# Kernel tuning notes

Hardware: AMD Instinct MI355X
Metric: run time of the kernel (lower is better)

The kernel has to match this reference:

```python
import jax, jax.numpy as jnp
import numpy as np
from jax import lax

K = 3            # kernel_size
PAD = (K - 1) // 2


def zero_insert_stride2(x):
    # tf_pad_with_stride for stride=2, f_conv!=1, padding='SAME':
    # interleave a zero BEFORE each element along W then H -> [b, 2h, 2w, c]
    b, h, w, c = x.shape
    z1 = jnp.zeros_like(x)
    med1 = jnp.stack([z1, x], axis=3).reshape(b, h, 2 * w, c)
    z2 = jnp.zeros_like(med1)
    return jnp.stack([z2, med1], axis=2).reshape(b, 2 * h, 2 * w, c)


def conv_valid(x, w):
    return lax.conv_general_dilated(
        x, w, window_strides=(1, 1), padding='VALID',
        dimension_numbers=('NHWC', 'HWIO', 'NHWC'))


def backward_conv(grad_output, inputs, kernels):
    p = PAD
    # --- grad w.r.t. input: zero-insert (stride 2), pad to FULL, conv with rot180(W)^T ---
    go = zero_insert_stride2(grad_output)                       # [B, 2h, 2w, Cout]
    fmt_inp = jnp.pad(go, ((0, 0), (p, p), (p, p), (0, 0)))     # tf_pad_to_full_conv2d (SAME)
    fmt_wt = jnp.transpose(kernels[::-1, ::-1], (0, 1, 3, 2))   # rot180 + swap I/O -> [k,k,Cout,Cin]
    grad_in = conv_valid(fmt_inp, fmt_wt)                       # [B, H, W, Cin]

    # --- grad w.r.t. weight: conv(inputs as batch-of-channels, grad_out as kernel) ---
    inp_pad = jnp.pad(inputs, ((0, 0), (p, p), (p, p), (0, 0)))  # SAME: pad inputs too
    fmt_inp2 = jnp.transpose(inp_pad, (3, 1, 2, 0))              # [Cin, H+2p, W+2p, B]
    fmt_wt2 = jnp.transpose(go, (1, 2, 0, 3))                    # NHWC->HWIO: [2h, 2w, B, Cout]
    gw = conv_valid(fmt_inp2, fmt_wt2)                           # [Cin, k, k, Cout]
    grad_wt = jnp.transpose(gw, (1, 2, 0, 3))                    # [k, k, Cin, Cout]

    # --- grad w.r.t. bias ---
    grad_bias = jnp.sum(grad_output, axis=(0, 1, 2))             # [Cout]
    return grad_in, grad_wt, grad_bias


def setup_inputs() -> dict:
    key = jax.random.key(0)
    k1, k2, k3 = jax.random.split(key, 3)
    grad_output = jax.random.normal(k1, (32, 28, 28, 256), dtype=jnp.float32)
    inputs = jax.random.normal(k2, (32, 56, 56, 256), dtype=jnp.float32)
    kernels = jax.random.normal(k3, (3, 3, 256, 256), dtype=jnp.float32)
    return {"grad_output": grad_output, "inputs": inputs, "kernels": kernels}


def reference(grad_output, inputs, kernels):
    return backward_conv(grad_output, inputs, kernels)
```

## Files before the change

### kernel.cpp

```cpp
#include <hip/hip_runtime.h>

#define Bn   32
#define HIN  56
#define WIN  56
#define Cc   256
#define HG   28
#define WG   28
#define NPIX (HG*WG)

#define GIN_SIZE (Bn*HIN*WIN*Cc)
#define GW_SIZE  (9*Cc*Cc)
#define GW_OFF   GIN_SIZE
#define BIAS_OFF (GW_OFF + GW_SIZE)

typedef short bf16x8 __attribute__((ext_vector_type(8)));
typedef float f32x4  __attribute__((ext_vector_type(4)));

__device__ __forceinline__ unsigned short f2bf(float f) {
    union { float f; unsigned int u; } v; v.f = f;
    unsigned int u = v.u;
    u += 0x7fffu + ((u >> 16) & 1u);
    return (unsigned short)(u >> 16);
}

__device__ __forceinline__ int swz(int row, int k) {
    int g2 = (k >> 3) ^ (row & 3) ^ ((row >> 2) & 3);
    return row * 32 + (g2 << 3) + (k & 7);
}

__device__ __forceinline__ int swz64(int row, int k) {
    int gq = ((k >> 3) ^ (row & 7) ^ ((row >> 4) & 7)) & 7;
    return row * 64 + (gq << 3) + (k & 7);
}

__global__ __launch_bounds__(256) void k_zero(float* __restrict__ p, int n) {
    int i = blockIdx.x * 256 + threadIdx.x;
    if (i < n) p[i] = 0.f;
}

__global__ __launch_bounds__(256) void k_grad_in(
    const float* __restrict__ g,
    const float* __restrict__ wt,
    float* __restrict__ out)
{
    __shared__ unsigned short ga[128 * 32];
    __shared__ unsigned short wb[128 * 32];

    const int t    = threadIdx.x;
    const int l    = t & 63;
    const int wave = t >> 6;
    const int mbase = (wave & 1) * 64;
    const int nbase = (wave >> 1) * 64;
    const int q    = l >> 4;
    const int r16  = l & 15;

    const int mtile = blockIdx.x;
    const int ntile = blockIdx.y;
    const int cls   = blockIdx.z;
    const int dy = cls >> 1, dx = cls & 1;

    const int sp = t >> 1;
    const int sc = (t & 1) * 16;
    const int P_s   = mtile * 128 + sp;
    const int b_s   = P_s / NPIX;
    const int rem_s = P_s % NPIX;
    const int iy_s  = rem_s / WG;
    const int jx_s  = rem_s % WG;
    const int sci   = ntile * 128 + sp;

    f32x4 acc[4][4];
    #pragma unroll
    for (int a = 0; a < 4; ++a)
        #pragma unroll
        for (int b = 0; b < 4; ++b) acc[a][b] = (f32x4){0.f, 0.f, 0.f, 0.f};

    int aoff[4], boff[4];
    #pragma unroll
    for (int mf = 0; mf < 4; ++mf) aoff[mf] = swz(mbase + mf * 16 + r16, q * 8);
    #pragma unroll
    for (int nf = 0; nf < 4; ++nf) boff[nf] = swz(nbase + nf * 16 + r16, q * 8);

    const int nky = dy ? 1 : 2;
    const int nkx = dx ? 1 : 2;

    for (int ty = 0; ty < nky; ++ty) {
        const int di   = dy ? 0 : (ty == 0 ? -1 : 0);
        const int krow = dy ? 1 : (ty == 0 ?  2 : 0);
        for (int tx = 0; tx < nkx; ++tx) {
            const int dj   = dx ? 0 : (tx == 0 ? -1 : 0);
            const int kcol = dx ? 1 : (tx == 0 ?  2 : 0);

            const int gi = iy_s + di, gj = jx_s + dj;
            const bool valid = (gi >= 0) && (gj >= 0);
            const float* __restrict__ gsrc = g + (size_t)((b_s * HG + gi) * WG + gj) * Cc + sc;
            const float* __restrict__ wsrc = wt + (size_t)((krow * 3 + kcol) * Cc + sci) * Cc + sc;

            #pragma unroll 1
            for (int co0 = 0; co0 < Cc; co0 += 32) {
                __syncthreads();
                {
                    float4 v0 = make_float4(0,0,0,0), v1 = v0, v2 = v0, v3 = v0;
                    if (valid) {
                        v0 = *(const float4*)(gsrc + co0 + 0);
                        v1 = *(const float4*)(gsrc + co0 + 4);
                        v2 = *(const float4*)(gsrc + co0 + 8);
                        v3 = *(const float4*)(gsrc + co0 + 12);
                    }
                    ushort4 u0 = {f2bf(v0.x), f2bf(v0.y), f2bf(v0.z), f2bf(v0.w)};
                    ushort4 u1 = {f2bf(v1.x), f2bf(v1.y), f2bf(v1.z), f2bf(v1.w)};
                    ushort4 u2 = {f2bf(v2.x), f2bf(v2.y), f2bf(v2.z), f2bf(v2.w)};
                    ushort4 u3 = {f2bf(v3.x), f2bf(v3.y), f2bf(v3.z), f2bf(v3.w)};
                    *(ushort4*)&ga[swz(sp, sc + 0)]  = u0;
                    *(ushort4*)&ga[swz(sp, sc + 4)]  = u1;
                    *(ushort4*)&ga[swz(sp, sc + 8)]  = u2;
                    *(ushort4*)&ga[swz(sp, sc + 12)] = u3;
                }
                {
                    float4 v0 = *(const float4*)(wsrc + co0 + 0);
                    float4 v1 = *(const float4*)(wsrc + co0 + 4);
                    float4 v2 = *(const float4*)(wsrc + co0 + 8);
                    float4 v3 = *(const float4*)(wsrc + co0 + 12);
                    ushort4 u0 = {f2bf(v0.x), f2bf(v0.y), f2bf(v0.z), f2bf(v0.w)};
                    ushort4 u1 = {f2bf(v1.x), f2bf(v1.y), f2bf(v1.z), f2bf(v1.w)};
                    ushort4 u2 = {f2bf(v2.x), f2bf(v2.y), f2bf(v2.z), f2bf(v2.w)};
                    ushort4 u3 = {f2bf(v3.x), f2bf(v3.y), f2bf(v3.z), f2bf(v3.w)};
                    *(ushort4*)&wb[swz(sp, sc + 0)]  = u0;
                    *(ushort4*)&wb[swz(sp, sc + 4)]  = u1;
                    *(ushort4*)&wb[swz(sp, sc + 8)]  = u2;
                    *(ushort4*)&wb[swz(sp, sc + 12)] = u3;
                }
                __syncthreads();

                bf16x8 af[4], bf[4];
                #pragma unroll
                for (int mf = 0; mf < 4; ++mf) af[mf] = *(const bf16x8*)&ga[aoff[mf]];
                #pragma unroll
                for (int nf = 0; nf < 4; ++nf) bf[nf] = *(const bf16x8*)&wb[boff[nf]];
                #pragma unroll
                for (int mf = 0; mf < 4; ++mf)
                    #pragma unroll
                    for (int nf = 0; nf < 4; ++nf)
                        acc[mf][nf] = __builtin_amdgcn_mfma_f32_16x16x32_bf16(
                            af[mf], bf[nf], acc[mf][nf], 0, 0, 0);
            }
        }
    }

    #pragma unroll
    for (int mf = 0; mf < 4; ++mf) {
        #pragma unroll
        for (int rr = 0; rr < 4; ++rr) {
            const int P   = mtile * 128 + mbase + mf * 16 + q * 4 + rr;
            const int b   = P / NPIX;
            const int rem = P % NPIX;
            const int iy  = rem / WG, jx = rem % WG;
            const int y = 2 * iy + dy, x = 2 * jx + dx;
            float* orow = out + (size_t)((b * HIN + y) * WIN + x) * Cc
                              + ntile * 128 + nbase + r16;
            #pragma unroll
            for (int nf = 0; nf < 4; ++nf) orow[nf * 16] = acc[mf][nf][rr];
        }
    }
}

__global__ __launch_bounds__(256) void k_grad_wt(
    const float* __restrict__ g,
    const float* __restrict__ inp,
    float* __restrict__ gw)
{
    __shared__ unsigned short xa[128 * 64];
    __shared__ unsigned short xg[128 * 64];

    const int t    = threadIdx.x;
    const int l    = t & 63;
    const int wave = t >> 6;
    const int mbase = (wave & 1) * 64;
    const int nbase = (wave >> 1) * 64;
    const int q    = l >> 4;
    const int r16  = l & 15;

    const int tci = (blockIdx.x >> 1) * 128;
    const int tco = (blockIdx.x & 1) * 128;
    const int tap = blockIdx.y;
    const int ki = tap / 3, kj = tap % 3;
    const int b  = blockIdx.z;

    const int pg = t >> 5;
    const int p0 = pg * 8;
    const int c4 = (t & 31) * 4;

    f32x4 acc[4][4];
    #pragma unroll
    for (int a = 0; a < 4; ++a)
        #pragma unroll
        for (int c = 0; c < 4; ++c) acc[a][c] = (f32x4){0.f, 0.f, 0.f, 0.f};

    int aoff[2][4], boff[2][4];
    #pragma unroll
    for (int kk = 0; kk < 2; ++kk) {
        #pragma unroll
        for (int mf = 0; mf < 4; ++mf) {
            aoff[kk][mf] = swz64(mbase + mf * 16 + r16, kk * 32 + q * 8);
            boff[kk][mf] = swz64(nbase + mf * 16 + r16, kk * 32 + q * 8);
        }
    }

    const float* __restrict__ gb = g   + (size_t)b * NPIX * Cc;
    const float* __restrict__ ib = inp + (size_t)b * HIN * WIN * Cc;

    #pragma unroll 1
    for (int cc = 0; cc < 13; ++cc) {
        __syncthreads();
        {
            bf16x8 wx[4];
            #pragma unroll
            for (int j = 0; j < 8; ++j) {
                const int p  = cc * 64 + p0 + j;
                const int i  = p / WG, jx = p % WG;
                const int r  = ki + 2 * i, s = kj + 2 * jx;
                const bool v = (p < NPIX) && (r < HIN) && (s < WIN);
                float4 xv = make_float4(0.f, 0.f, 0.f, 0.f);
                if (v) xv = *(const float4*)(ib + (size_t)(r * WIN + s) * Cc + tci + c4);
                wx[0][j] = (short)f2bf(xv.x);
                wx[1][j] = (short)f2bf(xv.y);
                wx[2][j] = (short)f2bf(xv.z);
                wx[3][j] = (short)f2bf(xv.w);
            }
            #pragma unroll
            for (int c = 0; c < 4; ++c)
                *(bf16x8*)&xa[swz64(c4 + c, p0)] = wx[c];
        }
        {
            bf16x8 wgv[4];
            #pragma unroll
            for (int j = 0; j < 8; ++j) {
                const int p  = cc * 64 + p0 + j;
                const bool v = (p < NPIX);
                float4 gv = make_float4(0.f, 0.f, 0.f, 0.f);
                if (v) gv = *(const float4*)(gb + (size_t)p * Cc + tco + c4);
                wgv[0][j] = (short)f2bf(gv.x);
                wgv[1][j] = (short)f2bf(gv.y);
                wgv[2][j] = (short)f2bf(gv.z);
                wgv[3][j] = (short)f2bf(gv.w);
            }
            #pragma unroll
            for (int c = 0; c < 4; ++c)
                *(bf16x8*)&xg[swz64(c4 + c, p0)] = wgv[c];
        }
        __syncthreads();

        #pragma unroll
        for (int kk = 0; kk < 2; ++kk) {
            bf16x8 af[4], bfr[4];
            #pragma unroll
            for (int mf = 0; mf < 4; ++mf) af[mf]  = *(const bf16x8*)&xa[aoff[kk][mf]];
            #pragma unroll
            for (int nf = 0; nf < 4; ++nf) bfr[nf] = *(const bf16x8*)&xg[boff[kk][nf]];
            #pragma unroll
            for (int mf = 0; mf < 4; ++mf)
                #pragma unroll
                for (int nf = 0; nf < 4; ++nf)
                    acc[mf][nf] = __builtin_amdgcn_mfma_f32_16x16x32_bf16(
                        af[mf], bfr[nf], acc[mf][nf], 0, 0, 0);
        }
    }

    #pragma unroll
    for (int mf = 0; mf < 4; ++mf) {
        #pragma unroll
        for (int rr = 0; rr < 4; ++rr) {
            const int cirow = tci + mbase + mf * 16 + q * 4 + rr;
            float* dst = gw + (size_t)(tap * Cc + cirow) * Cc + tco + nbase + r16;
            #pragma unroll
            for (int nf = 0; nf < 4; ++nf) atomicAdd(dst + nf * 16, acc[mf][nf][rr]);
        }
    }
}

__global__ __launch_bounds__(256) void k_bias(
    const float* __restrict__ g, float* __restrict__ bias)
{
    const int t = threadIdx.x;
    const float* base = g + (size_t)blockIdx.x * 256 * Cc;
    float acc = 0.f;
    #pragma unroll 8
    for (int p = 0; p < 256; ++p) acc += base[(size_t)p * Cc + t];
    atomicAdd(bias + t, acc);
}

extern "C" void kernel_launch(void* const* d_in, const int* in_sizes, int n_in,
                              void* d_out, int out_size, void* d_ws, size_t ws_size,
                              hipStream_t stream) {
    const float* g   = (const float*)d_in[0];
    const float* inp = (const float*)d_in[1];
    const float* wt  = (const float*)d_in[2];
    float* out = (float*)d_out;

    const int nzero = GW_SIZE + 256;
    k_zero<<<(nzero + 255) / 256, 256, 0, stream>>>(out + GW_OFF, nzero);
    k_grad_in<<<dim3(196, 2, 4), 256, 0, stream>>>(g, wt, out);
    k_grad_wt<<<dim3(4, 9, 32), 256, 0, stream>>>(g, inp, out + GW_OFF);
    k_bias<<<98, 256, 0, stream>>>(g, out + BIAS_OFF);
}
```

Baseline: 207.0 us.

## Register-prefetch next chunk during MFMA and use LDS-only barriers

Both GEMM kernels (grad-input and grad-weight) now load the next K-chunk from global memory into registers before the current chunk is written to LDS and consumed by MFMA, so global latency overlaps compute. The __syncthreads calls become a custom barrier that waits only on lgkmcnt, so in-flight global prefetch loads are not drained at each barrier. The float-to-bf16 conversion now uses the compiler's __bf16 cast instead of manual rounding, which may map to a hardware conversion instruction. The trade-off is higher register pressure from holding prefetched float4s, which could lower occupancy.

```diff
diff --git a/kernel.cpp b/kernel.cpp
--- a/kernel.cpp
+++ b/kernel.cpp
@@ -17,10 +17,13 @@
 typedef float f32x4  __attribute__((ext_vector_type(4)));
 
 __device__ __forceinline__ unsigned short f2bf(float f) {
-    union { float f; unsigned int u; } v; v.f = f;
-    unsigned int u = v.u;
-    u += 0x7fffu + ((u >> 16) & 1u);
-    return (unsigned short)(u >> 16);
+    return __builtin_bit_cast(unsigned short, (__bf16)f);
+}
+
+__device__ __forceinline__ void lds_barrier() {
+    asm volatile("s_waitcnt lgkmcnt(0)" ::: "memory");
+    __builtin_amdgcn_s_barrier();
+    asm volatile("" ::: "memory");
 }
 
 __device__ __forceinline__ int swz(int row, int k) {
@@ -95,41 +98,39 @@
             const float* __restrict__ gsrc = g + (size_t)((b_s * HG + gi) * WG + gj) * Cc + sc;
             const float* __restrict__ wsrc = wt + (size_t)((krow * 3 + kcol) * Cc + sci) * Cc + sc;
 
+            float4 av[4], bv[4];
+            #pragma unroll
+            for (int u = 0; u < 4; ++u) {
+                av[u] = make_float4(0.f, 0.f, 0.f, 0.f);
+                if (valid) av[u] = *(const float4*)(gsrc + u * 4);
+                bv[u] = *(const float4*)(wsrc + u * 4);
+            }
+
             #pragma unroll 1
             for (int co0 = 0; co0 < Cc; co0 += 32) {
-                __syncthreads();
-                {
-                    float4 v0 = make_float4(0,0,0,0), v1 = v0, v2 = v0, v3 = v0;
-                    if (valid) {
-                        v0 = *(const float4*)(gsrc + co0 + 0);
-                        v1 = *(const float4*)(gsrc + co0 + 4);
-                        v2 = *(const float4*)(gsrc + co0 + 8);
-                        v3 = *(const float4*)(gsrc + co0 + 12);
+                ushort4 ua[4], ub[4];
+                #pragma unroll
+                for (int u = 0; u < 4; ++u) {
+                    ua[u] = (ushort4){f2bf(av[u].x), f2bf(av[u].y), f2bf(av[u].z), f2bf(av[u].w)};
+                    ub[u] = (ushort4){f2bf(bv[u].x), f2bf(bv[u].y), f2bf(bv[u].z), f2bf(bv[u].w)};
+                }
+                if (co0 + 32 < Cc) {
+                    #pragma unroll
+                    for (int u = 0; u < 4; ++u) {
+                        float4 a2 = make_float4(0.f, 0.f, 0.f, 0.f);
+                        if (valid) a2 = *(const float4*)(gsrc + co0 + 32 + u * 4);
+                        float4 b2 = *(const float4*)(wsrc + co0 + 32 + u * 4);
+                        av[u] = a2;
+                        bv[u] = b2;
                     }
-                    ushort4 u0 = {f2bf(v0.x), f2bf(v0.y), f2bf(v0.z), f2bf(v0.w)};
-                    ushort4 u1 = {f2bf(v1.x), f2bf(v1.y), f2bf(v1.z), f2bf(v1.w)};
-                    ushort4 u2 = {f2bf(v2.x), f2bf(v2.y), f2bf(v2.z), f2bf(v2.w)};
-                    ushort4 u3 = {f2bf(v3.x), f2bf(v3.y), f2bf(v3.z), f2bf(v3.w)};
-                    *(ushort4*)&ga[swz(sp, sc + 0)]  = u0;
-                    *(ushort4*)&ga[swz(sp, sc + 4)]  = u1;
-                    *(ushort4*)&ga[swz(sp, sc + 8)]  = u2;
-                    *(ushort4*)&ga[swz(sp, sc + 12)] = u3;
                 }
-                {
-                    float4 v0 = *(const float4*)(wsrc + co0 + 0);
-                    float4 v1 = *(const float4*)(wsrc + co0 + 4);
-                    float4 v2 = *(const float4*)(wsrc + co0 + 8);
-                    float4 v3 = *(const float4*)(wsrc + co0 + 12);
-                    ushort4 u0 = {f2bf(v0.x), f2bf(v0.y), f2bf(v0.z), f2bf(v0.w)};
-                    ushort4 u1 = {f2bf(v1.x), f2bf(v1.y), f2bf(v1.z), f2bf(v1.w)};
-                    ushort4 u2 = {f2bf(v2.x), f2bf(v2.y), f2bf(v2.z), f2bf(v2.w)};
-                    ushort4 u3 = {f2bf(v3.x), f2bf(v3.y), f2bf(v3.z), f2bf(v3.w)};
-                    *(ushort4*)&wb[swz(sp, sc + 0)]  = u0;
-                    *(ushort4*)&wb[swz(sp, sc + 4)]  = u1;
-                    *(ushort4*)&wb[swz(sp, sc + 8)]  = u2;
-                    *(ushort4*)&wb[swz(sp, sc + 12)] = u3;
+                lds_barrier();
+                #pragma unroll
+                for (int u = 0; u < 4; ++u) {
+                    *(ushort4*)&ga[swz(sp, sc + u * 4)] = ua[u];
+                    *(ushort4*)&wb[swz(sp, sc + u * 4)] = ub[u];
                 }
-                __syncthreads();
+                lds_barrier();
 
                 bf16x8 af[4], bf[4];
                 #pragma unroll
@@ -208,46 +209,50 @@
     const float* __restrict__ gb = g   + (size_t)b * NPIX * Cc;
     const float* __restrict__ ib = inp + (size_t)b * HIN * WIN * Cc;
 
+    float4 xr[8], gr[8];
+
+    auto load_chunk = [&](int cc) {
+        #pragma unroll
+        for (int j = 0; j < 8; ++j) {
+            const int p  = cc * 64 + p0 + j;
+            const int i  = p / WG, jw = p % WG;
+            const int r  = ki + 2 * i, s = kj + 2 * jw;
+            const bool vx = (p < NPIX) && (r < HIN) && (s < WIN);
+            const bool vg = (p < NPIX);
+            float4 xv = make_float4(0.f, 0.f, 0.f, 0.f);
+            float4 gv = make_float4(0.f, 0.f, 0.f, 0.f);
+            if (vx) xv = *(const float4*)(ib + (size_t)(r * WIN + s) * Cc + tci + c4);
+            if (vg) gv = *(const float4*)(gb + (size_t)p * Cc + tco + c4);
+            xr[j] = xv;
+            gr[j] = gv;
+        }
+    };
+
+    load_chunk(0);
+
     #pragma unroll 1
     for (int cc = 0; cc < 13; ++cc) {
-        __syncthreads();
-        {
-            bf16x8 wx[4];
-            #pragma unroll
-            for (int j = 0; j < 8; ++j) {
-                const int p  = cc * 64 + p0 + j;
-                const int i  = p / WG, jx = p % WG;
-                const int r  = ki + 2 * i, s = kj + 2 * jx;
-                const bool v = (p < NPIX) && (r < HIN) && (s < WIN);
-                float4 xv = make_float4(0.f, 0.f, 0.f, 0.f);
-                if (v) xv = *(const float4*)(ib + (size_t)(r * WIN + s) * Cc + tci + c4);
-                wx[0][j] = (short)f2bf(xv.x);
-                wx[1][j] = (short)f2bf(xv.y);
-                wx[2][j] = (short)f2bf(xv.z);
-                wx[3][j] = (short)f2bf(xv.w);
-            }
-            #pragma unroll
-            for (int c = 0; c < 4; ++c)
-                *(bf16x8*)&xa[swz64(c4 + c, p0)] = wx[c];
-        }
-        {
-            bf16x8 wgv[4];
-            #pragma unroll
-            for (int j = 0; j < 8; ++j) {
-                const int p  = cc * 64 + p0 + j;
-                const bool v = (p < NPIX);
-                float4 gv = make_float4(0.f, 0.f, 0.f, 0.f);
-                if (v) gv = *(const float4*)(gb + (size_t)p * Cc + tco + c4);
-                wgv[0][j] = (short)f2bf(gv.x);
-                wgv[1][j] = (short)f2bf(gv.y);
-                wgv[2][j] = (short)f2bf(gv.z);
-                wgv[3][j] = (short)f2bf(gv.w);
-            }
-            #pragma unroll
-            for (int c = 0; c < 4; ++c)
-                *(bf16x8*)&xg[swz64(c4 + c, p0)] = wgv[c];
-        }
-        __syncthreads();
+        bf16x8 wx[4], wg[4];
+        #pragma unroll
+        for (int j = 0; j < 8; ++j) {
+            wx[0][j] = (short)f2bf(xr[j].x);
+            wx[1][j] = (short)f2bf(xr[j].y);
+            wx[2][j] = (short)f2bf(xr[j].z);
+            wx[3][j] = (short)f2bf(xr[j].w);
+            wg[0][j] = (short)f2bf(gr[j].x);
+            wg[1][j] = (short)f2bf(gr[j].y);
+            wg[2][j] = (short)f2bf(gr[j].z);
+            wg[3][j] = (short)f2bf(gr[j].w);
+        }
+        if (cc + 1 < 13) load_chunk(cc + 1);
+
+        lds_barrier();
+        #pragma unroll
+        for (int c = 0; c < 4; ++c) {
+            *(bf16x8*)&xa[swz64(c4 + c, p0)] = wx[c];
+            *(bf16x8*)&xg[swz64(c4 + c, p0)] = wg[c];
+        }
+        lds_barrier();
 
         #pragma unroll
         for (int kk = 0; kk < 2; ++kk) {
```

Measured after the change: 227.9 us. 10.1% more time.
